# Optimization experiments

Measured on AMD Instinct MI355X. Metric: run time of the kernel, lower is better.

Reference implementation:

```python
import jax, jax.numpy as jnp
import numpy as np

STATE_DIM = 5
HIDDEN = 32
B, S = 128, 4096
D_IN = STATE_DIM + 1 + 3  # [h_prev, temp_seq, direction]


def setup_inputs() -> dict:
    key = jax.random.key(0)
    ks = jax.random.split(key, 16)
    g = lambda k, shp: (jax.random.normal(k, shp, dtype=jnp.float32) * 0.1)
    z = lambda shp: jnp.zeros(shp, jnp.float32)
    inp = {}
    inp["h_prev"] = jax.random.normal(ks[0], (B, S, STATE_DIM), dtype=jnp.float32)
    inp["delta_x"] = jax.random.uniform(ks[1], (B, S, 6), dtype=jnp.float32)
    # internal layer 0 (input D_IN -> HIDDEN), layer 1 (HIDDEN -> HIDDEN)
    inp["Wa0"] = g(ks[2], (D_IN, HIDDEN)); inp["ba0"] = z((HIDDEN,))
    inp["Wb0"] = g(ks[3], (D_IN, HIDDEN)); inp["bb0"] = z((HIDDEN,))
    inp["Wa1"] = g(ks[4], (HIDDEN, HIDDEN)); inp["ba1"] = z((HIDDEN,))
    inp["Wb1"] = g(ks[5], (HIDDEN, HIDDEN)); inp["bb1"] = z((HIDDEN,))
    inp["W_alpha"] = g(ks[6], (HIDDEN, 1)); inp["b_alpha"] = z((1,))
    inp["W_beta"]  = g(ks[7], (HIDDEN, 1)); inp["b_beta"]  = z((1,))
    inp["W_gamma"] = g(ks[8], (HIDDEN, 1)); inp["b_gamma"] = z((1,))
    inp["W_c"] = g(ks[9], (HIDDEN, STATE_DIM)); inp["b_c"] = z((STATE_DIM,))
    inp["W_out"] = g(ks[10], (STATE_DIM, 1))  # no bias
    return inp


def reference(h_prev, delta_x, Wa0, ba0, Wb0, bb0, Wa1, ba1, Wb1, bb1,
              W_alpha, b_alpha, W_beta, b_beta, W_gamma, b_gamma,
              W_c, b_c, W_out):
    # delta_x: [delta_strain, delta_time, delta_temp, init_strain, init_time, init_temp]
    df = delta_x[..., :3]                       # (B, S, 3)
    init_temp = delta_x[:, 0:1, 5:6]            # (B, 1, 1) init temp at t=0
    temp_seq = jnp.cumsum(delta_x[..., 2:3], axis=1) + init_temp  # (B, S, 1)
    # normalized increment direction
    norm = jnp.maximum(jnp.sqrt(jnp.sum(df * df, axis=-1, keepdims=True)), 1e-7)
    direction = df / norm                       # (B, S, 3)
    l = jnp.concatenate([h_prev, temp_seq, direction], axis=-1)   # (B, S, 9)
    # two internal tanh*tanh gated dense layers
    l = jnp.tanh(l @ Wa0 + ba0) * jnp.tanh(l @ Wb0 + bb0)         # (B, S, 32)
    l = jnp.tanh(l @ Wa1 + ba1) * jnp.tanh(l @ Wb1 + bb1)         # (B, S, 32)
    # exp gates (non-negative rate params)
    alpha = jnp.exp(l @ W_alpha + b_alpha)      # (B, S, 1)
    beta  = jnp.exp(l @ W_beta  + b_beta)
    gamma = jnp.exp(l @ W_gamma + b_gamma)
    c_n = jnp.tanh(l @ W_c + b_c)               # (B, S, 5)
    # update gate from physical increments
    z = 1.0 - jnp.exp(-alpha * jnp.abs(df[..., 0:1])
                      - beta * df[..., 1:2]
                      - gamma * jnp.abs(df[..., 2:3]))
    h_n = (1.0 - z) * h_prev + z * c_n          # (B, S, 5)
    sigma_n = h_n @ W_out                       # (B, S, 1)
    return (h_n, sigma_n)
```

## Files before the change

### kernel.cpp

```cpp
#include <hip/hip_runtime.h>

#define B_DIMC   128
#define S_DIMC   4096
#define N_TOK    (B_DIMC * S_DIMC)
#define CHUNK    256
#define N_CHUNK  (N_TOK / CHUNK)
#define CPB      (S_DIMC / CHUNK)

typedef __attribute__((ext_vector_type(8))) short  short8;
typedef __attribute__((ext_vector_type(4))) float  floatx4;
typedef __attribute__((ext_vector_type(4))) int    intx4;

__device__ float g_chunksums[N_CHUNK];

__device__ __forceinline__ unsigned short f2bf(float f) {
    unsigned u = __builtin_bit_cast(unsigned, f);
    u = (u + 0x7FFFu + ((u >> 16) & 1u)) >> 16;
    return (unsigned short)u;
}
__device__ __forceinline__ int packbf(float a, float b) {
    return (int)f2bf(a) | ((int)f2bf(b) << 16);
}
__device__ __forceinline__ float fast_tanh(float x) {
    float e = __builtin_amdgcn_exp2f(2.885390082f * __builtin_amdgcn_fmed3f(x, -9.0f, 9.0f));
    return fmaf(-2.0f, __builtin_amdgcn_rcpf(e + 1.0f), 1.0f);
}
__device__ __forceinline__ float gate2(float a, float b) {
    const float c = 2.885390082f;
    float ea = __builtin_amdgcn_exp2f(c * __builtin_amdgcn_fmed3f(a, -9.0f, 9.0f));
    float eb = __builtin_amdgcn_exp2f(c * __builtin_amdgcn_fmed3f(b, -9.0f, 9.0f));
    float t  = fmaf(ea, eb, 1.0f);
    float u  = ea + eb;
    return (t - u) * __builtin_amdgcn_rcpf(t + u);
}

__global__ __launch_bounds__(256) void chunksum_kernel(const float* __restrict__ dx) {
    const int t    = blockIdx.x * CHUNK + threadIdx.x;
    const int lane = threadIdx.x & 63;
    const int wid  = threadIdx.x >> 6;
    __shared__ float wsum[4];
    float x = dx[(size_t)t * 6 + 2];
    #pragma unroll
    for (int off = 32; off >= 1; off >>= 1) x += __shfl_down(x, off, 64);
    if (lane == 0) wsum[wid] = x;
    __syncthreads();
    if (threadIdx.x == 0)
        g_chunksums[blockIdx.x] = wsum[0] + wsum[1] + wsum[2] + wsum[3];
}

__device__ __forceinline__ float head_w(int n, int k,
                                        const float* Wal, const float* Wbe,
                                        const float* Wga, const float* Wc) {
    if (n == 0) return Wal[k];
    if (n == 1) return Wbe[k];
    if (n == 2) return Wga[k];
    if (n < 8)  return Wc[k * 5 + (n - 3)];
    return 0.0f;
}

union SMemU {
    struct {
        short W[4][32][40];
        short Wh[16][40];
        float Bias[16];
    } b;
    short A[4][64][40];
};

__global__ __launch_bounds__(256) void msc_kernel(
    const float* __restrict__ h_prev, const float* __restrict__ dx,
    const float* __restrict__ Wa0, const float* __restrict__ ba0,
    const float* __restrict__ Wb0, const float* __restrict__ bb0,
    const float* __restrict__ Wa1, const float* __restrict__ ba1,
    const float* __restrict__ Wb1, const float* __restrict__ bb1,
    const float* __restrict__ W_alpha, const float* __restrict__ b_alpha,
    const float* __restrict__ W_beta,  const float* __restrict__ b_beta,
    const float* __restrict__ W_gamma, const float* __restrict__ b_gamma,
    const float* __restrict__ W_c,     const float* __restrict__ b_c,
    const float* __restrict__ W_out,
    float* __restrict__ out)
{
    __shared__ __align__(16) SMemU sm;
    __shared__ __align__(16) float sTemps[4][64];
    __shared__ float sWsum[4];

    const int tid  = threadIdx.x;
    const int w    = tid >> 6;
    const int lane = tid & 63;
    const int n    = lane & 15;
    const int quad = lane >> 4;
    const int t    = blockIdx.x * CHUNK + tid;

    const float* hp = h_prev + (size_t)t * 5;
    const float* d  = dx     + (size_t)t * 6;
    const float hp0 = hp[0], hp1 = hp[1], hp2 = hp[2], hp3 = hp[3], hp4 = hp[4];
    const float df0 = d[0], df1 = d[1], df2 = d[2];

    const int batch = blockIdx.x / CPB;
    const int cib   = blockIdx.x % CPB;
    float cs = (lane < cib) ? g_chunksums[batch * CPB + lane] : 0.0f;
    #pragma unroll
    for (int m = 1; m < 64; m <<= 1) cs += __shfl_xor(cs, m, 64);
    const float coff = dx[(size_t)batch * S_DIMC * 6 + 5] + cs;

    float w5a[2], w5b[2], bA0[2], bB0[2], bA1[2], bB1[2];
    #pragma unroll
    for (int nt = 0; nt < 2; ++nt) {
        const int col = nt * 16 + n;
        w5a[nt] = Wa0[5 * 32 + col];  w5b[nt] = Wb0[5 * 32 + col];
        bA0[nt] = ba0[col];           bB0[nt] = bb0[col];
        bA1[nt] = ba1[col];           bB1[nt] = bb1[col];
    }

    float x = df2;
    #pragma unroll
    for (int off = 1; off < 64; off <<= 1) {
        float y = __shfl_up(x, off, 64);
        if (lane >= off) x += y;
    }
    if (lane == 63) sWsum[w] = x;

    #pragma unroll
    for (int m = 0; m < 4; ++m) {
        const float* Wsrc = (m == 0) ? Wa0 : (m == 1) ? Wb0 : (m == 2) ? Wa1 : Wb1;
        const bool l0 = (m < 2);
        #pragma unroll
        for (int dd = tid; dd < 512; dd += 256) {
            const int col = dd >> 4, kd = dd & 15, k0 = kd * 2, k1 = k0 + 1;
            float v0, v1;
            if (l0) {
                v0 = (k0 < 9 && k0 != 5) ? Wsrc[k0 * 32 + col] : 0.0f;
                v1 = (k1 < 9 && k1 != 5) ? Wsrc[k1 * 32 + col] : 0.0f;
            } else {
                v0 = Wsrc[k0 * 32 + col];
                v1 = Wsrc[k1 * 32 + col];
            }
            ((int*)&sm.b.W[m][col][0])[kd] = packbf(v0, v1);
        }
    }
    {
        const int hn = tid >> 4, kd = tid & 15, k0 = kd * 2;
        const float v0 = head_w(hn, k0,     W_alpha, W_beta, W_gamma, W_c);
        const float v1 = head_w(hn, k0 + 1, W_alpha, W_beta, W_gamma, W_c);
        ((int*)&sm.b.Wh[hn][0])[kd] = packbf(v0, v1);
    }
    if (tid < 16) {
        sm.b.Bias[tid] = (tid == 0) ? b_alpha[0] : (tid == 1) ? b_beta[0]
                       : (tid == 2) ? b_gamma[0] : (tid < 8) ? b_c[tid - 3] : 0.0f;
    }

    __syncthreads();

    short8 Ba0f[2], Bb0f[2], Ba1f[2], Bb1f[2], Bhf;
    #pragma unroll
    for (int nt = 0; nt < 2; ++nt) {
        const int col = nt * 16 + n;
        Ba0f[nt] = *(const short8*)&sm.b.W[0][col][quad * 8];
        Bb0f[nt] = *(const short8*)&sm.b.W[1][col][quad * 8];
        Ba1f[nt] = *(const short8*)&sm.b.W[2][col][quad * 8];
        Bb1f[nt] = *(const short8*)&sm.b.W[3][col][quad * 8];
    }
    Bhf = *(const short8*)&sm.b.Wh[n][quad * 8];
    const float hbias = sm.b.Bias[n];

    float pre = coff;
    if (w > 0) pre += sWsum[0];
    if (w > 1) pre += sWsum[1];
    if (w > 2) pre += sWsum[2];
    const float temp_t = pre + x;

    __syncthreads();

    sTemps[w][lane] = temp_t;

    const float nrm = fmaxf(sqrtf(df0*df0 + df1*df1 + df2*df2), 1e-7f);
    const float inv = __builtin_amdgcn_rcpf(nrm);
    {
        int* arow = (int*)&sm.A[w][lane][0];
        intx4 v0 = { packbf(hp0, hp1), packbf(hp2, hp3),
                     packbf(hp4, 0.0f), packbf(df0*inv, df1*inv) };
        intx4 v1 = { packbf(df2*inv, 0.0f), 0, 0, 0 };
        intx4 z  = { 0, 0, 0, 0 };
        *(intx4*)&arow[0]  = v0;
        *(intx4*)&arow[4]  = v1;
        *(intx4*)&arow[8]  = z;
        *(intx4*)&arow[12] = z;
    }

    #pragma unroll
    for (int mt = 0; mt < 4; ++mt) {
        const short8  Af = *(const short8*)&sm.A[w][mt * 16 + n][quad * 8];
        const floatx4 tv = *(const floatx4*)&sTemps[w][mt * 16 + quad * 4];
        #pragma unroll
        for (int nt = 0; nt < 2; ++nt) {
            floatx4 Ca, Cb;
            #pragma unroll
            for (int r = 0; r < 4; ++r) {
                Ca[r] = fmaf(tv[r], w5a[nt], bA0[nt]);
                Cb[r] = fmaf(tv[r], w5b[nt], bB0[nt]);
            }
            Ca = __builtin_amdgcn_mfma_f32_16x16x32_bf16(Af, Ba0f[nt], Ca, 0, 0, 0);
            Cb = __builtin_amdgcn_mfma_f32_16x16x32_bf16(Af, Bb0f[nt], Cb, 0, 0, 0);
            #pragma unroll
            for (int r = 0; r < 4; ++r)
                sm.A[w][mt * 16 + quad * 4 + r][nt * 16 + n] = (short)f2bf(gate2(Ca[r], Cb[r]));
        }
    }

    #pragma unroll
    for (int mt = 0; mt < 4; ++mt) {
        const short8 Af = *(const short8*)&sm.A[w][mt * 16 + n][quad * 8];
        #pragma unroll
        for (int nt = 0; nt < 2; ++nt) {
            floatx4 Ca = { bA1[nt], bA1[nt], bA1[nt], bA1[nt] };
            floatx4 Cb = { bB1[nt], bB1[nt], bB1[nt], bB1[nt] };
            Ca = __builtin_amdgcn_mfma_f32_16x16x32_bf16(Af, Ba1f[nt], Ca, 0, 0, 0);
            Cb = __builtin_amdgcn_mfma_f32_16x16x32_bf16(Af, Bb1f[nt], Cb, 0, 0, 0);
            #pragma unroll
            for (int r = 0; r < 4; ++r)
                sm.A[w][mt * 16 + quad * 4 + r][nt * 16 + n] = (short)f2bf(gate2(Ca[r], Cb[r]));
        }
    }

    short8 Ah[4];
    #pragma unroll
    for (int mt = 0; mt < 4; ++mt)
        Ah[mt] = *(const short8*)&sm.A[w][mt * 16 + n][quad * 8];
    __syncthreads();

    float* hc = (float*)&sm.A[w][0][0];
    #pragma unroll
    for (int mt = 0; mt < 4; ++mt) {
        floatx4 C = { hbias, hbias, hbias, hbias };
        C = __builtin_amdgcn_mfma_f32_16x16x32_bf16(Ah[mt], Bhf, C, 0, 0, 0);
        if (n < 8) {
            #pragma unroll
            for (int r = 0; r < 4; ++r)
                hc[(mt * 16 + quad * 4 + r) * 12 + n] = C[r];
        }
    }

    const floatx4 h0v = *(const floatx4*)&hc[lane * 12];
    const floatx4 h1v = *(const floatx4*)&hc[lane * 12 + 4];

    const float alpha = __expf(h0v[0]);
    const float beta  = __expf(h0v[1]);
    const float gamma = __expf(h0v[2]);
    const float z     = 1.0f - __expf(-(alpha * fabsf(df0) + beta * df1 + gamma * fabsf(df2)));
    const float omz   = 1.0f - z;

    const float c0 = fast_tanh(h0v[3]), c1 = fast_tanh(h1v[0]), c2 = fast_tanh(h1v[1]),
                c3 = fast_tanh(h1v[2]), c4 = fast_tanh(h1v[3]);

    const float hn0 = omz * hp0 + z * c0;
    const float hn1 = omz * hp1 + z * c1;
    const float hn2 = omz * hp2 + z * c2;
    const float hn3 = omz * hp3 + z * c3;
    const float hn4 = omz * hp4 + z * c4;

    float* out_h = out + (size_t)t * 5;
    out_h[0] = hn0; out_h[1] = hn1; out_h[2] = hn2; out_h[3] = hn3; out_h[4] = hn4;
    out[(size_t)N_TOK * 5 + t] =
        hn0 * W_out[0] + hn1 * W_out[1] + hn2 * W_out[2] + hn3 * W_out[3] + hn4 * W_out[4];
}

extern "C" void kernel_launch(void* const* d_in, const int* in_sizes, int n_in,
                              void* d_out, int out_size, void* d_ws, size_t ws_size,
                              hipStream_t stream) {
    const float* h_prev  = (const float*)d_in[0];
    const float* dx      = (const float*)d_in[1];
    const float* Wa0     = (const float*)d_in[2];
    const float* ba0     = (const float*)d_in[3];
    const float* Wb0     = (const float*)d_in[4];
    const float* bb0     = (const float*)d_in[5];
    const float* Wa1     = (const float*)d_in[6];
    const float* ba1     = (const float*)d_in[7];
    const float* Wb1     = (const float*)d_in[8];
    const float* bb1     = (const float*)d_in[9];
    const float* W_alpha = (const float*)d_in[10];
    const float* b_alpha = (const float*)d_in[11];
    const float* W_beta  = (const float*)d_in[12];
    const float* b_beta  = (const float*)d_in[13];
    const float* W_gamma = (const float*)d_in[14];
    const float* b_gamma = (const float*)d_in[15];
    const float* W_c     = (const float*)d_in[16];
    const float* b_c     = (const float*)d_in[17];
    const float* W_out   = (const float*)d_in[18];
    float* out = (float*)d_out;

    chunksum_kernel<<<N_CHUNK, CHUNK, 0, stream>>>(dx);
    msc_kernel<<<N_CHUNK, CHUNK, 0, stream>>>(
        h_prev, dx,
        Wa0, ba0, Wb0, bb0, Wa1, ba1, Wb1, bb1,
        W_alpha, b_alpha, W_beta, b_beta, W_gamma, b_gamma,
        W_c, b_c, W_out, out);
}
```

Baseline: 133.6 us.

## Use hardware bf16 pack, vectorize chunksum loads, trim syncs and shared memory

Swaps the software round-to-bf16 for the v_cvt_pk_bf16_f32 instruction. The chunk-sum kernel now reads float4 vectors and picks out the temperature column, where it used to do strided scalar loads. The main kernel stores temperatures in spare columns of the A tile, which removes the separate sTemps array and shrinks shared memory. It also shortens the prefix shuffle reduction to 16 lanes, replaces a block-wide barrier with compiler fences because each wave only touches its own region, and requests 8 blocks per CU in launch bounds. The risks are register pressure from the occupancy hint and reliance on wave-local ordering without a barrier.

```diff
diff --git a/kernel.cpp b/kernel.cpp
--- a/kernel.cpp
+++ b/kernel.cpp
@@ -13,14 +13,13 @@
 
 __device__ float g_chunksums[N_CHUNK];
 
-__device__ __forceinline__ unsigned short f2bf(float f) {
-    unsigned u = __builtin_bit_cast(unsigned, f);
-    u = (u + 0x7FFFu + ((u >> 16) & 1u)) >> 16;
-    return (unsigned short)u;
-}
-__device__ __forceinline__ int packbf(float a, float b) {
-    return (int)f2bf(a) | ((int)f2bf(b) << 16);
-}
+__device__ __forceinline__ int cvtpk(float a, float b) {
+    int r;
+    asm("v_cvt_pk_bf16_f32 %0, %1, %2" : "=v"(r) : "v"(a), "v"(b));
+    return r;
+}
+__device__ __forceinline__ short bf1(float a) { return (short)cvtpk(a, a); }
+
 __device__ __forceinline__ float fast_tanh(float x) {
     float e = __builtin_amdgcn_exp2f(2.885390082f * __builtin_amdgcn_fmed3f(x, -9.0f, 9.0f));
     return fmaf(-2.0f, __builtin_amdgcn_rcpf(e + 1.0f), 1.0f);
@@ -35,14 +34,21 @@
 }
 
 __global__ __launch_bounds__(256) void chunksum_kernel(const float* __restrict__ dx) {
-    const int t    = blockIdx.x * CHUNK + threadIdx.x;
     const int lane = threadIdx.x & 63;
     const int wid  = threadIdx.x >> 6;
     __shared__ float wsum[4];
-    float x = dx[(size_t)t * 6 + 2];
-    #pragma unroll
-    for (int off = 32; off >= 1; off >>= 1) x += __shfl_down(x, off, 64);
-    if (lane == 0) wsum[wid] = x;
+    const float* base = dx + (size_t)blockIdx.x * (CHUNK * 6);
+    float s = 0.0f;
+    #pragma unroll
+    for (int j = threadIdx.x; j < 384; j += 256) {
+        const float4 v = *(const float4*)(base + j * 4);
+        const int r = j % 3;
+        if (r == 0) s += v.z;
+        if (r == 2) s += v.x;
+    }
+    #pragma unroll
+    for (int off = 32; off >= 1; off >>= 1) s += __shfl_down(s, off, 64);
+    if (lane == 0) wsum[wid] = s;
     __syncthreads();
     if (threadIdx.x == 0)
         g_chunksums[blockIdx.x] = wsum[0] + wsum[1] + wsum[2] + wsum[3];
@@ -63,11 +69,12 @@
         short W[4][32][40];
         short Wh[16][40];
         float Bias[16];
+        float Wsum[4];
     } b;
     short A[4][64][40];
 };
 
-__global__ __launch_bounds__(256) void msc_kernel(
+__global__ __launch_bounds__(256, 8) void msc_kernel(
     const float* __restrict__ h_prev, const float* __restrict__ dx,
     const float* __restrict__ Wa0, const float* __restrict__ ba0,
     const float* __restrict__ Wb0, const float* __restrict__ bb0,
@@ -81,8 +88,6 @@
     float* __restrict__ out)
 {
     __shared__ __align__(16) SMemU sm;
-    __shared__ __align__(16) float sTemps[4][64];
-    __shared__ float sWsum[4];
 
     const int tid  = threadIdx.x;
     const int w    = tid >> 6;
@@ -99,9 +104,13 @@
     const int batch = blockIdx.x / CPB;
     const int cib   = blockIdx.x % CPB;
     float cs = (lane < cib) ? g_chunksums[batch * CPB + lane] : 0.0f;
-    #pragma unroll
-    for (int m = 1; m < 64; m <<= 1) cs += __shfl_xor(cs, m, 64);
-    const float coff = dx[(size_t)batch * S_DIMC * 6 + 5] + cs;
+    cs += __shfl_xor(cs, 1, 64);
+    cs += __shfl_xor(cs, 2, 64);
+    cs += __shfl_xor(cs, 4, 64);
+    cs += __shfl_xor(cs, 8, 64);
+    const float csum = __builtin_bit_cast(float,
+        __builtin_amdgcn_readfirstlane(__builtin_bit_cast(int, cs)));
+    const float coff = dx[(size_t)batch * S_DIMC * 6 + 5] + csum;
 
     float w5a[2], w5b[2], bA0[2], bB0[2], bA1[2], bB1[2];
     #pragma unroll
@@ -118,7 +127,7 @@
         float y = __shfl_up(x, off, 64);
         if (lane >= off) x += y;
     }
-    if (lane == 63) sWsum[w] = x;
+    if (lane == 63) sm.b.Wsum[w] = x;
 
     #pragma unroll
     for (int m = 0; m < 4; ++m) {
@@ -135,14 +144,14 @@
                 v0 = Wsrc[k0 * 32 + col];
                 v1 = Wsrc[k1 * 32 + col];
             }
-            ((int*)&sm.b.W[m][col][0])[kd] = packbf(v0, v1);
+            ((int*)&sm.b.W[m][col][0])[kd] = cvtpk(v0, v1);
         }
     }
     {
         const int hn = tid >> 4, kd = tid & 15, k0 = kd * 2;
         const float v0 = head_w(hn, k0,     W_alpha, W_beta, W_gamma, W_c);
         const float v1 = head_w(hn, k0 + 1, W_alpha, W_beta, W_gamma, W_c);
-        ((int*)&sm.b.Wh[hn][0])[kd] = packbf(v0, v1);
+        ((int*)&sm.b.Wh[hn][0])[kd] = cvtpk(v0, v1);
     }
     if (tid < 16) {
         sm.b.Bias[tid] = (tid == 0) ? b_alpha[0] : (tid == 1) ? b_beta[0]
@@ -164,33 +173,36 @@
     const float hbias = sm.b.Bias[n];
 
     float pre = coff;
-    if (w > 0) pre += sWsum[0];
-    if (w > 1) pre += sWsum[1];
-    if (w > 2) pre += sWsum[2];
+    if (w > 0) pre += sm.b.Wsum[0];
+    if (w > 1) pre += sm.b.Wsum[1];
+    if (w > 2) pre += sm.b.Wsum[2];
     const float temp_t = pre + x;
 
     __syncthreads();
-
-    sTemps[w][lane] = temp_t;
 
     const float nrm = fmaxf(sqrtf(df0*df0 + df1*df1 + df2*df2), 1e-7f);
     const float inv = __builtin_amdgcn_rcpf(nrm);
     {
         int* arow = (int*)&sm.A[w][lane][0];
-        intx4 v0 = { packbf(hp0, hp1), packbf(hp2, hp3),
-                     packbf(hp4, 0.0f), packbf(df0*inv, df1*inv) };
-        intx4 v1 = { packbf(df2*inv, 0.0f), 0, 0, 0 };
-        intx4 z  = { 0, 0, 0, 0 };
+        intx4 v0 = { cvtpk(hp0, hp1), cvtpk(hp2, hp3),
+                     cvtpk(hp4, 0.0f), cvtpk(df0*inv, df1*inv) };
+        intx4 v1 = { cvtpk(df2*inv, 0.0f), 0, 0, 0 };
+        intx4 z4 = { 0, 0, 0, 0 };
         *(intx4*)&arow[0]  = v0;
         *(intx4*)&arow[4]  = v1;
-        *(intx4*)&arow[8]  = z;
-        *(intx4*)&arow[12] = z;
+        *(intx4*)&arow[8]  = z4;
+        *(intx4*)&arow[12] = z4;
+        *(float*)&arow[16] = temp_t;
     }
 
     #pragma unroll
     for (int mt = 0; mt < 4; ++mt) {
-        const short8  Af = *(const short8*)&sm.A[w][mt * 16 + n][quad * 8];
-        const floatx4 tv = *(const floatx4*)&sTemps[w][mt * 16 + quad * 4];
+        const short8 Af = *(const short8*)&sm.A[w][mt * 16 + n][quad * 8];
+        const int rb = mt * 16 + quad * 4;
+        floatx4 tv;
+        #pragma unroll
+        for (int r = 0; r < 4; ++r)
+            tv[r] = *(const float*)&sm.A[w][rb + r][32];
         #pragma unroll
         for (int nt = 0; nt < 2; ++nt) {
             floatx4 Ca, Cb;
@@ -203,7 +215,7 @@
             Cb = __builtin_amdgcn_mfma_f32_16x16x32_bf16(Af, Bb0f[nt], Cb, 0, 0, 0);
             #pragma unroll
             for (int r = 0; r < 4; ++r)
-                sm.A[w][mt * 16 + quad * 4 + r][nt * 16 + n] = (short)f2bf(gate2(Ca[r], Cb[r]));
+                sm.A[w][mt * 16 + quad * 4 + r][nt * 16 + n] = bf1(gate2(Ca[r], Cb[r]));
         }
     }
 
@@ -218,7 +230,7 @@
             Cb = __builtin_amdgcn_mfma_f32_16x16x32_bf16(Af, Bb1f[nt], Cb, 0, 0, 0);
             #pragma unroll
             for (int r = 0; r < 4; ++r)
-                sm.A[w][mt * 16 + quad * 4 + r][nt * 16 + n] = (short)f2bf(gate2(Ca[r], Cb[r]));
+                sm.A[w][mt * 16 + quad * 4 + r][nt * 16 + n] = bf1(gate2(Ca[r], Cb[r]));
         }
     }
 
@@ -226,7 +238,7 @@
     #pragma unroll
     for (int mt = 0; mt < 4; ++mt)
         Ah[mt] = *(const short8*)&sm.A[w][mt * 16 + n][quad * 8];
-    __syncthreads();
+    asm volatile("" ::: "memory");
 
     float* hc = (float*)&sm.A[w][0][0];
     #pragma unroll
@@ -239,6 +251,7 @@
                 hc[(mt * 16 + quad * 4 + r) * 12 + n] = C[r];
         }
     }
+    asm volatile("" ::: "memory");
 
     const floatx4 h0v = *(const floatx4*)&hc[lane * 12];
     const floatx4 h1v = *(const floatx4*)&hc[lane * 12 + 4];
```

Result: slower. 148.9 us (+11.4%).
